# Kernel optimization log

Hardware: AMD Instinct MI355X
Metric: run time of the kernel (lower is better)

Reference implementation:

```python
import jax, jax.numpy as jnp
import numpy as np

N_NODES = 50000
N_EDGES = 800000
IN_CH = 64
HID = 128  # hidden_dim_conv == hidden_dim_readout


def setup_inputs() -> dict:
    key = jax.random.key(0)
    ks = jax.random.split(key, 16)
    x = jax.random.normal(ks[0], (N_NODES, 1, IN_CH), dtype=jnp.float32)
    edge_index = jax.random.randint(ks[1], (2, N_EDGES), 0, N_NODES, dtype=jnp.int64)
    edge_weight = jax.random.uniform(ks[2], (N_EDGES,), dtype=jnp.float32)

    def lin(k, out_d, in_d):
        s = 1.0 / np.sqrt(in_d)
        return jax.random.uniform(k, (out_d, in_d), minval=-s, maxval=s, dtype=jnp.float32)

    params = {
        "W_rel0": lin(ks[3], HID, IN_CH), "b_rel0": jnp.zeros((HID,), jnp.float32),
        "W_root0": lin(ks[4], HID, IN_CH),
        "W_ro0": lin(ks[5], HID, HID), "b_ro0": jnp.zeros((HID,), jnp.float32),
        "W_rel1": lin(ks[6], HID, HID), "b_rel1": jnp.zeros((HID,), jnp.float32),
        "W_root1": lin(ks[7], HID, HID),
        "W_ro1": lin(ks[8], HID, HID), "b_ro1": jnp.zeros((HID,), jnp.float32),
        "W_prd": lin(ks[9], 1, HID), "b_prd": jnp.zeros((1,), jnp.float32),
    }
    return {"dynamic_node_features": x, "edge_index": edge_index, "edge_weight": edge_weight, **params}


def reference(dynamic_node_features, edge_index, edge_weight,
              W_rel0, b_rel0, W_root0, W_ro0, b_ro0,
              W_rel1, b_rel1, W_root1, W_ro1, b_ro1,
              W_prd, b_prd):
    # Dropout layers are identity at inference.
    src, dst = edge_index[0], edge_index[1]
    n = dynamic_node_features.shape[0]
    # in-degree counts for 'mean' aggregation (nodes with no in-edges -> 0 output)
    counts = jax.ops.segment_sum(jnp.ones((edge_weight.shape[0],), edge_weight.dtype), dst, num_segments=n)
    denom = jnp.maximum(counts, 1.0)[:, None]  # [N,1]

    def graph_conv(h, W_rel, b_rel, W_root):
        # PyG GraphConv: lin_rel(mean_j edge_weight_ij * h_j) + lin_root(h_i)
        msg = edge_weight[:, None] * h[src]                       # [E,C]
        agg = jax.ops.segment_sum(msg, dst, num_segments=n) / denom  # [N,C]
        return agg @ W_rel.T + b_rel + h @ W_root.T

    h = dynamic_node_features[:, 0, :]                            # [N,IN_CH]
    h = jax.nn.relu(graph_conv(h, W_rel0, b_rel0, W_root0))
    h = jax.nn.relu(h @ W_ro0.T + b_ro0)                          # readout layer 0
    h = jax.nn.relu(graph_conv(h, W_rel1, b_rel1, W_root1))
    h = jax.nn.relu(h @ W_ro1.T + b_ro1)                          # readout layer 1
    out = h @ W_prd.T + b_prd                                     # [N,1]
    return out[:, None, :]                                        # [N,1,1]
```

## Files before the change

### kernel.cpp

```cpp
#include <hip/hip_runtime.h>
#include <hip/hip_fp16.h>

#define N_NODES 50000
#define N_EDGES 800000
#define IN_CH 64
#define HID 128
#define MAXDEG 64

typedef __attribute__((ext_vector_type(8))) short bf16x8;
typedef __attribute__((ext_vector_type(4))) float f32x4;

__device__ __forceinline__ unsigned pack_split(float v) {
    unsigned u = __float_as_uint(v);
    unsigned hi = (u + 0x7fffu + ((u >> 16) & 1u)) & 0xffff0000u;
    float r = v - __uint_as_float(hi);
    unsigned ur = __float_as_uint(r);
    unsigned lo = ((ur + 0x7fffu + ((ur >> 16) & 1u)) >> 16) & 0xffffu;
    return hi | lo;
}


__global__ __launch_bounds__(256) void count_fill_pack(
    const int* __restrict__ src, const int* __restrict__ dst,
    const float* __restrict__ w, int* __restrict__ cnt, int2* __restrict__ csr, int e,
    const float* __restrict__ x, unsigned* __restrict__ xp, __half* __restrict__ xh, int nx,
    const float* __restrict__ w_rel0, const float* __restrict__ w_root0,
    const float* __restrict__ w_ro0, const float* __restrict__ w_rel1,
    const float* __restrict__ w_root1, const float* __restrict__ w_ro1,
    unsigned short* __restrict__ hi, unsigned short* __restrict__ lo) {
    int tid = blockIdx.x * blockDim.x + threadIdx.x;
    int i8 = tid * 8;
    if (i8 + 7 < e) {
        int4 d0 = *(const int4*)&dst[i8];
        int4 d1 = *(const int4*)&dst[i8 + 4];
        int4 s0 = *(const int4*)&src[i8];
        int4 s1 = *(const int4*)&src[i8 + 4];
        float4 w0 = *(const float4*)&w[i8];
        float4 w1 = *(const float4*)&w[i8 + 4];
        int dd[8] = {d0.x, d0.y, d0.z, d0.w, d1.x, d1.y, d1.z, d1.w};
        int ss[8] = {s0.x, s0.y, s0.z, s0.w, s1.x, s1.y, s1.z, s1.w};
        float ww[8] = {w0.x, w0.y, w0.z, w0.w, w1.x, w1.y, w1.z, w1.w};
        int rr[8];
#pragma unroll
        for (int q = 0; q < 8; ++q) rr[q] = atomicAdd(&cnt[dd[q]], 1);
#pragma unroll
        for (int q = 0; q < 8; ++q) {
            if (rr[q] < MAXDEG) {
                unsigned long long v =
                    ((unsigned long long)(unsigned)__float_as_uint(ww[q]) << 32) | (unsigned)ss[q];
                __builtin_nontemporal_store(
                    v, (unsigned long long*)&csr[(size_t)dd[q] * MAXDEG + rr[q]]);
            }
        }
    } else if (i8 < e) {
        for (int i = i8; i < e; ++i) {
            int d = dst[i];
            int r = atomicAdd(&cnt[d], 1);
            if (r < MAXDEG) {
                unsigned long long v =
                    ((unsigned long long)(unsigned)__float_as_uint(w[i]) << 32) | (unsigned)src[i];
                __builtin_nontemporal_store(
                    v, (unsigned long long*)&csr[(size_t)d * MAXDEG + r]);
            }
        }
    }
    if (tid < nx) {
        float v = x[tid];
        xp[tid] = pack_split(v);
        xh[tid] = __float2half(v);
    }
    if (tid < 81920) {
        const float* srcw;
        int li;
        if (tid < 8192) { srcw = w_rel0; li = tid; }
        else if (tid < 16384) { srcw = w_root0; li = tid - 8192; }
        else if (tid < 32768) { srcw = w_ro0; li = tid - 16384; }
        else if (tid < 49152) { srcw = w_rel1; li = tid - 32768; }
        else if (tid < 65536) { srcw = w_root1; li = tid - 49152; }
        else { srcw = w_ro1; li = tid - 65536; }
        unsigned p = pack_split(srcw[li]);
        hi[tid] = (unsigned short)(p >> 16);
        lo[tid] = (unsigned short)(p & 0xffffu);
    }
}


template <int T, int ROW_STRIDE>
__device__ __forceinline__ void agg_tier_h2(const __half2* __restrict__ h2,
                                            const int2* __restrict__ cp,
                                            int& e, int end, int sl,
                                            float& ax, float& ay) {
    for (; e + T <= end; e += T) {
        int2 p[T];
        __half2 v[T];
#pragma unroll
        for (int q = 0; q < T; ++q) p[q] = cp[e + q];
#pragma unroll
        for (int q = 0; q < T; ++q) v[q] = h2[(size_t)p[q].x * ROW_STRIDE + sl];
#pragma unroll
        for (int q = 0; q < T; ++q) {
            float wv = __int_as_float(p[q].y);
            float2 f = __half22float2(v[q]);
            ax += wv * f.x;
            ay += wv * f.y;
        }
    }
}

__global__ void aggregate64(const __half2* __restrict__ xh2, const int* __restrict__ cnt,
                            const int2* __restrict__ csr,
                            unsigned* __restrict__ agg, int n) {
    int tid = blockIdx.x * blockDim.x + threadIdx.x;
    int lane = tid & 63;
    int half = lane >> 5;
    int sl = lane & 31;
    int node = ((tid >> 6) << 1) + half;
    if (node >= n) return;
    int deg = cnt[node];
    int end = deg < MAXDEG ? deg : MAXDEG;
    float inv = 1.0f / fmaxf((float)deg, 1.0f);
    const int2* cp = csr + (size_t)node * MAXDEG;
    float ax = 0.0f, ay = 0.0f;
    int e = 0;
    agg_tier_h2<16, 32>(xh2, cp, e, end, sl, ax, ay);
    agg_tier_h2<8, 32>(xh2, cp, e, end, sl, ax, ay);
    agg_tier_h2<4, 32>(xh2, cp, e, end, sl, ax, ay);
    agg_tier_h2<1, 32>(xh2, cp, e, end, sl, ax, ay);
    uint2 o;
    o.x = pack_split(ax * inv);
    o.y = pack_split(ay * inv);
    ((uint2*)agg)[(size_t)node * 32 + sl] = o;
}

__global__ void aggregate128(const __half2* __restrict__ h2h, const int* __restrict__ cnt,
                             const int2* __restrict__ csr,
                             unsigned* __restrict__ agg, int n) {
    int lane = threadIdx.x & 63;
    int node = (int)((blockIdx.x * blockDim.x + threadIdx.x) >> 6);
    if (node >= n) return;
    node = __builtin_amdgcn_readfirstlane(node);
    int deg = cnt[node];
    int end = deg < MAXDEG ? deg : MAXDEG;
    float inv = 1.0f / fmaxf((float)deg, 1.0f);
    const int2* cp = csr + (size_t)node * MAXDEG;
    float ax = 0.0f, ay = 0.0f;
    int e = 0;
    agg_tier_h2<16, 64>(h2h, cp, e, end, lane, ax, ay);
    agg_tier_h2<8, 64>(h2h, cp, e, end, lane, ax, ay);
    agg_tier_h2<4, 64>(h2h, cp, e, end, lane, ax, ay);
    agg_tier_h2<1, 64>(h2h, cp, e, end, lane, ax, ay);
    uint2 o;
    o.x = pack_split(ax * inv);
    o.y = pack_split(ay * inv);
    ((uint2*)agg)[(size_t)node * 64 + lane] = o;
}


template <int K, int NMAT, bool RELU, int EMIT>
__global__ __launch_bounds__(256, 2) void gemm_mfma(
    const unsigned* __restrict__ A0,
    const unsigned short* __restrict__ W0Hi, const unsigned short* __restrict__ W0Lo,
    const unsigned* __restrict__ A1,
    const unsigned short* __restrict__ W1Hi, const unsigned short* __restrict__ W1Lo,
    const float* __restrict__ bias, void* __restrict__ Yv, __half* __restrict__ Yh,
    const float* __restrict__ pred_w, const float* __restrict__ pred_b,
    float* __restrict__ pred_out, int n) {
    constexpr int KS = K / 32;
    const int lane = (int)threadIdx.x & 63;
    const int wv = (int)threadIdx.x >> 6;
    const int col = lane & 15;
    const int quad = lane >> 4;

    bf16x8 wh[NMAT][2][KS], wl[NMAT][2][KS];
#pragma unroll
    for (int m = 0; m < NMAT; ++m) {
        const unsigned short* Whi = m ? W1Hi : W0Hi;
        const unsigned short* Wlo = m ? W1Lo : W0Lo;
#pragma unroll
        for (int tt = 0; tt < 2; ++tt) {
            const int j = (2 * wv + tt) * 16 + col;
#pragma unroll
            for (int ks = 0; ks < KS; ++ks) {
                const size_t wo = (size_t)j * K + ks * 32 + quad * 8;
                wh[m][tt][ks] = *(const bf16x8*)&Whi[wo];
                wl[m][tt][ks] = *(const bf16x8*)&Wlo[wo];
            }
        }
    }

    float bb[2], wpv[2];
#pragma unroll
    for (int tt = 0; tt < 2; ++tt) {
        bb[tt] = bias[(2 * wv + tt) * 16 + col];
        if constexpr (EMIT == 2) wpv[tt] = pred_w[(2 * wv + tt) * 16 + col];
    }

    const int ngroups = (n + 15) >> 4;
    for (int g = (int)blockIdx.x; g < ngroups; g += (int)gridDim.x) {
        const int m0 = g * 16;
        int arow = m0 + col;
        if (arow >= n) arow = n - 1;

        f32x4 acc[2];
#pragma unroll
        for (int tt = 0; tt < 2; ++tt) acc[tt] = (f32x4){0.f, 0.f, 0.f, 0.f};

#pragma unroll
        for (int m = 0; m < NMAT; ++m) {
            const unsigned* Ap = m ? A1 : A0;
#pragma unroll
            for (int ks = 0; ks < KS; ++ks) {
                const unsigned* ap = &Ap[(size_t)arow * K + ks * 32 + quad * 8];
                uint4 q0 = *(const uint4*)ap;
                uint4 q1 = *(const uint4*)(ap + 4);
                bf16x8 ahi, alo;
                ahi[0] = (short)(q0.x >> 16); alo[0] = (short)(q0.x & 0xffffu);
                ahi[1] = (short)(q0.y >> 16); alo[1] = (short)(q0.y & 0xffffu);
                ahi[2] = (short)(q0.z >> 16); alo[2] = (short)(q0.z & 0xffffu);
                ahi[3] = (short)(q0.w >> 16); alo[3] = (short)(q0.w & 0xffffu);
                ahi[4] = (short)(q1.x >> 16); alo[4] = (short)(q1.x & 0xffffu);
                ahi[5] = (short)(q1.y >> 16); alo[5] = (short)(q1.y & 0xffffu);
                ahi[6] = (short)(q1.z >> 16); alo[6] = (short)(q1.z & 0xffffu);
                ahi[7] = (short)(q1.w >> 16); alo[7] = (short)(q1.w & 0xffffu);
#pragma unroll
                for (int tt = 0; tt < 2; ++tt) {
                    acc[tt] = __builtin_amdgcn_mfma_f32_16x16x32_bf16(ahi, wh[m][tt][ks], acc[tt], 0, 0, 0);
                    acc[tt] = __builtin_amdgcn_mfma_f32_16x16x32_bf16(ahi, wl[m][tt][ks], acc[tt], 0, 0, 0);
                    acc[tt] = __builtin_amdgcn_mfma_f32_16x16x32_bf16(alo, wh[m][tt][ks], acc[tt], 0, 0, 0);
                }
            }
        }

        float yv[2][4];
#pragma unroll
        for (int tt = 0; tt < 2; ++tt)
#pragma unroll
            for (int r = 0; r < 4; ++r) {
                float y = acc[tt][r] + bb[tt];
                if (RELU) y = fmaxf(y, 0.f);
                yv[tt][r] = y;
            }

        if constexpr (EMIT != 2) {
#pragma unroll
            for (int tt = 0; tt < 2; ++tt) {
                const int j = (2 * wv + tt) * 16 + col;
#pragma unroll
                for (int r = 0; r < 4; ++r) {
                    int node = m0 + quad * 4 + r;
                    if (node >= n) continue;
                    ((unsigned*)Yv)[(size_t)node * 128 + j] = pack_split(yv[tt][r]);
                    if constexpr (EMIT == 1)
                        Yh[(size_t)node * 128 + j] = __float2half(yv[tt][r]);
                }
            }
        } else {
            __shared__ float pp[4][16];
            float pr[4];
#pragma unroll
            for (int r = 0; r < 4; ++r) pr[r] = yv[0][r] * wpv[0] + yv[1][r] * wpv[1];
#pragma unroll
            for (int off = 8; off > 0; off >>= 1)
#pragma unroll
                for (int r = 0; r < 4; ++r) pr[r] += __shfl_down(pr[r], off);
            if (col == 0) {
#pragma unroll
                for (int r = 0; r < 4; ++r) pp[wv][quad * 4 + r] = pr[r];
            }
            __syncthreads();
            if (wv == 0 && lane < 16) {
                int node = m0 + lane;
                if (node < n)
                    pred_out[node] = pp[0][lane] + pp[1][lane] + pp[2][lane] + pp[3][lane] + pred_b[0];
            }
            __syncthreads();
        }
    }
}


extern "C" void kernel_launch(void* const* d_in, const int* in_sizes, int n_in,
                              void* d_out, int out_size, void* d_ws, size_t ws_size,
                              hipStream_t stream) {
    const float* x = (const float*)d_in[0];
    const int* edge_index = (const int*)d_in[1];
    const float* edge_w = (const float*)d_in[2];
    const float* W_rel0 = (const float*)d_in[3];
    const float* b_rel0 = (const float*)d_in[4];
    const float* W_root0 = (const float*)d_in[5];
    const float* W_ro0 = (const float*)d_in[6];
    const float* b_ro0 = (const float*)d_in[7];
    const float* W_rel1 = (const float*)d_in[8];
    const float* b_rel1 = (const float*)d_in[9];
    const float* W_root1 = (const float*)d_in[10];
    const float* W_ro1 = (const float*)d_in[11];
    const float* b_ro1 = (const float*)d_in[12];
    const float* W_prd = (const float*)d_in[13];
    const float* b_prd = (const float*)d_in[14];
    float* out = (float*)d_out;

    const int* e_src = edge_index;
    const int* e_dst = edge_index + N_EDGES;

    char* ws = (char*)d_ws;
    size_t off = 0;
    auto alloc = [&](size_t bytes) {
        char* p = ws + off;
        off += (bytes + 255) & ~(size_t)255;
        return p;
    };
    int* cnt = (int*)alloc(N_NODES * 4);
    int2* csr = (int2*)alloc((size_t)N_NODES * MAXDEG * 8);
    unsigned short* WHI = (unsigned short*)alloc(81920 * 2);
    unsigned short* WLO = (unsigned short*)alloc(81920 * 2);
    unsigned* xp = (unsigned*)alloc((size_t)N_NODES * 64 * 4);
    __half* xh = (__half*)alloc((size_t)N_NODES * 64 * 2);
    unsigned* AGGp = (unsigned*)alloc((size_t)N_NODES * 128 * 4);
    unsigned* B1p = (unsigned*)alloc((size_t)N_NODES * 128 * 4);
    unsigned* B2p = (unsigned*)alloc((size_t)N_NODES * 128 * 4);
    __half* H2h = (__half*)alloc((size_t)N_NODES * 128 * 2);

    hipMemsetAsync(cnt, 0, N_NODES * 4, stream);

    const int NX = N_NODES * 64;
    count_fill_pack<<<(NX + 255) / 256, 256, 0, stream>>>(
        e_src, e_dst, edge_w, cnt, csr, N_EDGES,
        x, xp, xh, NX, W_rel0, W_root0, W_ro0, W_rel1, W_root1, W_ro1, WHI, WLO);

    const int AGGB64 = (((N_NODES + 1) / 2) * 64 + 255) / 256;
    const int AGGB = (N_NODES * 64 + 255) / 256;
    const int GGRID = 512;

    aggregate64<<<AGGB64, 256, 0, stream>>>((const __half2*)xh, cnt, csr, AGGp, N_NODES);
    gemm_mfma<64, 2, true, 0><<<GGRID, 256, 0, stream>>>(
        AGGp, WHI + 0, WLO + 0, xp, WHI + 8192, WLO + 8192, b_rel0,
        B1p, nullptr, nullptr, nullptr, nullptr, N_NODES);
    gemm_mfma<128, 1, true, 1><<<GGRID, 256, 0, stream>>>(
        B1p, WHI + 16384, WLO + 16384, nullptr, nullptr, nullptr, b_ro0,
        B2p, H2h, nullptr, nullptr, nullptr, N_NODES);
    aggregate128<<<AGGB, 256, 0, stream>>>((const __half2*)H2h, cnt, csr, AGGp, N_NODES);
    gemm_mfma<128, 2, true, 0><<<GGRID, 256, 0, stream>>>(
        AGGp, WHI + 32768, WLO + 32768, B2p, WHI + 49152, WLO + 49152, b_rel1,
        B1p, nullptr, nullptr, nullptr, nullptr, N_NODES);
    gemm_mfma<128, 1, true, 2><<<GGRID, 256, 0, stream>>>(
        B1p, WHI + 65536, WLO + 65536, nullptr, nullptr, nullptr, b_ro1,
        nullptr, nullptr, W_prd, b_prd, out, N_NODES);
}
```

Before: 291.7 us.

## Fuse graph-conv GEMM with readout GEMM via LDS and halve aggregate128 lanes

Each graph-conv GEMM and the readout GEMM that follows it now run in one kernel. The ReLU'd intermediate for each 16-row tile is written to shared memory in hi/lo split form and fed straight into a second MFMA pass, which removes the B1 round trip to global memory and two launches. aggregate128 now uses 32 lanes per node with 8-byte half loads and four accumulators, and its tier unrolling is simplified. The trade-offs are higher register pressure, since the second weight set stays resident and the min-blocks launch bound is dropped, plus extra block barriers per tile.

```diff
diff --git a/kernel.cpp b/kernel.cpp
--- a/kernel.cpp
+++ b/kernel.cpp
@@ -85,36 +85,13 @@
 }
 
 
-template <int T, int ROW_STRIDE>
-__device__ __forceinline__ void agg_tier_h2(const __half2* __restrict__ h2,
-                                            const int2* __restrict__ cp,
-                                            int& e, int end, int sl,
-                                            float& ax, float& ay) {
-    for (; e + T <= end; e += T) {
-        int2 p[T];
-        __half2 v[T];
-#pragma unroll
-        for (int q = 0; q < T; ++q) p[q] = cp[e + q];
-#pragma unroll
-        for (int q = 0; q < T; ++q) v[q] = h2[(size_t)p[q].x * ROW_STRIDE + sl];
-#pragma unroll
-        for (int q = 0; q < T; ++q) {
-            float wv = __int_as_float(p[q].y);
-            float2 f = __half22float2(v[q]);
-            ax += wv * f.x;
-            ay += wv * f.y;
-        }
-    }
-}
-
 __global__ void aggregate64(const __half2* __restrict__ xh2, const int* __restrict__ cnt,
                             const int2* __restrict__ csr,
                             unsigned* __restrict__ agg, int n) {
     int tid = blockIdx.x * blockDim.x + threadIdx.x;
     int lane = tid & 63;
-    int half = lane >> 5;
     int sl = lane & 31;
-    int node = ((tid >> 6) << 1) + half;
+    int node = ((tid >> 6) << 1) + (lane >> 5);
     if (node >= n) return;
     int deg = cnt[node];
     int end = deg < MAXDEG ? deg : MAXDEG;
@@ -122,56 +99,124 @@
     const int2* cp = csr + (size_t)node * MAXDEG;
     float ax = 0.0f, ay = 0.0f;
     int e = 0;
-    agg_tier_h2<16, 32>(xh2, cp, e, end, sl, ax, ay);
-    agg_tier_h2<8, 32>(xh2, cp, e, end, sl, ax, ay);
-    agg_tier_h2<4, 32>(xh2, cp, e, end, sl, ax, ay);
-    agg_tier_h2<1, 32>(xh2, cp, e, end, sl, ax, ay);
+    for (; e + 16 <= end; e += 16) {
+        int2 p[16];
+        __half2 v[16];
+#pragma unroll
+        for (int q = 0; q < 16; ++q) p[q] = cp[e + q];
+#pragma unroll
+        for (int q = 0; q < 16; ++q) v[q] = xh2[(size_t)p[q].x * 32 + sl];
+#pragma unroll
+        for (int q = 0; q < 16; ++q) {
+            float wv = __int_as_float(p[q].y);
+            float2 f = __half22float2(v[q]);
+            ax += wv * f.x;
+            ay += wv * f.y;
+        }
+    }
+    for (; e + 4 <= end; e += 4) {
+        int2 p[4];
+        __half2 v[4];
+#pragma unroll
+        for (int q = 0; q < 4; ++q) p[q] = cp[e + q];
+#pragma unroll
+        for (int q = 0; q < 4; ++q) v[q] = xh2[(size_t)p[q].x * 32 + sl];
+#pragma unroll
+        for (int q = 0; q < 4; ++q) {
+            float wv = __int_as_float(p[q].y);
+            float2 f = __half22float2(v[q]);
+            ax += wv * f.x;
+            ay += wv * f.y;
+        }
+    }
+    for (; e < end; ++e) {
+        int2 p = cp[e];
+        float wv = __int_as_float(p.y);
+        float2 f = __half22float2(xh2[(size_t)p.x * 32 + sl]);
+        ax += wv * f.x;
+        ay += wv * f.y;
+    }
     uint2 o;
     o.x = pack_split(ax * inv);
     o.y = pack_split(ay * inv);
     ((uint2*)agg)[(size_t)node * 32 + sl] = o;
 }
 
-__global__ void aggregate128(const __half2* __restrict__ h2h, const int* __restrict__ cnt,
+__global__ void aggregate128(const uint2* __restrict__ h2h, const int* __restrict__ cnt,
                              const int2* __restrict__ csr,
                              unsigned* __restrict__ agg, int n) {
-    int lane = threadIdx.x & 63;
-    int node = (int)((blockIdx.x * blockDim.x + threadIdx.x) >> 6);
+    int tid = blockIdx.x * blockDim.x + threadIdx.x;
+    int lane = tid & 63;
+    int sl = lane & 31;
+    int node = ((tid >> 6) << 1) + (lane >> 5);
     if (node >= n) return;
-    node = __builtin_amdgcn_readfirstlane(node);
     int deg = cnt[node];
     int end = deg < MAXDEG ? deg : MAXDEG;
     float inv = 1.0f / fmaxf((float)deg, 1.0f);
     const int2* cp = csr + (size_t)node * MAXDEG;
-    float ax = 0.0f, ay = 0.0f;
+    float ax = 0.0f, ay = 0.0f, az = 0.0f, aw = 0.0f;
     int e = 0;
-    agg_tier_h2<16, 64>(h2h, cp, e, end, lane, ax, ay);
-    agg_tier_h2<8, 64>(h2h, cp, e, end, lane, ax, ay);
-    agg_tier_h2<4, 64>(h2h, cp, e, end, lane, ax, ay);
-    agg_tier_h2<1, 64>(h2h, cp, e, end, lane, ax, ay);
-    uint2 o;
+    for (; e + 8 <= end; e += 8) {
+        int2 p[8];
+        uint2 v[8];
+#pragma unroll
+        for (int q = 0; q < 8; ++q) p[q] = cp[e + q];
+#pragma unroll
+        for (int q = 0; q < 8; ++q) v[q] = h2h[(size_t)p[q].x * 32 + sl];
+#pragma unroll
+        for (int q = 0; q < 8; ++q) {
+            float wv = __int_as_float(p[q].y);
+            float2 f0 = __half22float2(*(const __half2*)&v[q].x);
+            float2 f1 = __half22float2(*(const __half2*)&v[q].y);
+            ax += wv * f0.x;
+            ay += wv * f0.y;
+            az += wv * f1.x;
+            aw += wv * f1.y;
+        }
+    }
+    for (; e < end; ++e) {
+        int2 p = cp[e];
+        float wv = __int_as_float(p.y);
+        uint2 v = h2h[(size_t)p.x * 32 + sl];
+        float2 f0 = __half22float2(*(const __half2*)&v.x);
+        float2 f1 = __half22float2(*(const __half2*)&v.y);
+        ax += wv * f0.x;
+        ay += wv * f0.y;
+        az += wv * f1.x;
+        aw += wv * f1.y;
+    }
+    uint4 o;
     o.x = pack_split(ax * inv);
     o.y = pack_split(ay * inv);
-    ((uint2*)agg)[(size_t)node * 64 + lane] = o;
-}
-
-
-template <int K, int NMAT, bool RELU, int EMIT>
-__global__ __launch_bounds__(256, 2) void gemm_mfma(
+    o.z = pack_split(az * inv);
+    o.w = pack_split(aw * inv);
+    *(uint4*)&agg[(size_t)node * 128 + sl * 4] = o;
+}
+
+
+template <int K1, int NMAT, int EMIT2>
+__global__ __launch_bounds__(256) void gemm_fused(
     const unsigned* __restrict__ A0,
     const unsigned short* __restrict__ W0Hi, const unsigned short* __restrict__ W0Lo,
     const unsigned* __restrict__ A1,
     const unsigned short* __restrict__ W1Hi, const unsigned short* __restrict__ W1Lo,
-    const float* __restrict__ bias, void* __restrict__ Yv, __half* __restrict__ Yh,
+    const float* __restrict__ bias1,
+    const unsigned short* __restrict__ W2Hi, const unsigned short* __restrict__ W2Lo,
+    const float* __restrict__ bias2,
+    void* __restrict__ Yv, __half* __restrict__ Yh,
     const float* __restrict__ pred_w, const float* __restrict__ pred_b,
     float* __restrict__ pred_out, int n) {
-    constexpr int KS = K / 32;
+    constexpr int KS1 = K1 / 32;
+    constexpr int KS2 = 128 / 32;
     const int lane = (int)threadIdx.x & 63;
     const int wv = (int)threadIdx.x >> 6;
     const int col = lane & 15;
     const int quad = lane >> 4;
 
-    bf16x8 wh[NMAT][2][KS], wl[NMAT][2][KS];
+    __shared__ unsigned h1s[16][132];
+    __shared__ float pp[4][16];
+
+    bf16x8 wh1[NMAT][2][KS1], wl1[NMAT][2][KS1];
 #pragma unroll
     for (int m = 0; m < NMAT; ++m) {
         const unsigned short* Whi = m ? W1Hi : W0Hi;
@@ -180,19 +225,31 @@
         for (int tt = 0; tt < 2; ++tt) {
             const int j = (2 * wv + tt) * 16 + col;
 #pragma unroll
-            for (int ks = 0; ks < KS; ++ks) {
-                const size_t wo = (size_t)j * K + ks * 32 + quad * 8;
-                wh[m][tt][ks] = *(const bf16x8*)&Whi[wo];
-                wl[m][tt][ks] = *(const bf16x8*)&Wlo[wo];
-            }
-        }
-    }
-
-    float bb[2], wpv[2];
+            for (int ks = 0; ks < KS1; ++ks) {
+                const size_t wo = (size_t)j * K1 + ks * 32 + quad * 8;
+                wh1[m][tt][ks] = *(const bf16x8*)&Whi[wo];
+                wl1[m][tt][ks] = *(const bf16x8*)&Wlo[wo];
+            }
+        }
+    }
+    bf16x8 wh2[2][KS2], wl2[2][KS2];
 #pragma unroll
     for (int tt = 0; tt < 2; ++tt) {
-        bb[tt] = bias[(2 * wv + tt) * 16 + col];
-        if constexpr (EMIT == 2) wpv[tt] = pred_w[(2 * wv + tt) * 16 + col];
+        const int j = (2 * wv + tt) * 16 + col;
+#pragma unroll
+        for (int ks = 0; ks < KS2; ++ks) {
+            const size_t wo = (size_t)j * 128 + ks * 32 + quad * 8;
+            wh2[tt][ks] = *(const bf16x8*)&W2Hi[wo];
+            wl2[tt][ks] = *(const bf16x8*)&W2Lo[wo];
+        }
+    }
+
+    float bb1[2], bb2[2], wpv[2];
+#pragma unroll
+    for (int tt = 0; tt < 2; ++tt) {
+        bb1[tt] = bias1[(2 * wv + tt) * 16 + col];
+        bb2[tt] = bias2[(2 * wv + tt) * 16 + col];
+        if constexpr (EMIT2 == 2) wpv[tt] = pred_w[(2 * wv + tt) * 16 + col];
     }
 
     const int ngroups = (n + 15) >> 4;
@@ -204,13 +261,12 @@
         f32x4 acc[2];
 #pragma unroll
         for (int tt = 0; tt < 2; ++tt) acc[tt] = (f32x4){0.f, 0.f, 0.f, 0.f};
-
 #pragma unroll
         for (int m = 0; m < NMAT; ++m) {
             const unsigned* Ap = m ? A1 : A0;
 #pragma unroll
-            for (int ks = 0; ks < KS; ++ks) {
-                const unsigned* ap = &Ap[(size_t)arow * K + ks * 32 + quad * 8];
+            for (int ks = 0; ks < KS1; ++ks) {
+                const unsigned* ap = &Ap[(size_t)arow * K1 + ks * 32 + quad * 8];
                 uint4 q0 = *(const uint4*)ap;
                 uint4 q1 = *(const uint4*)(ap + 4);
                 bf16x8 ahi, alo;
@@ -224,24 +280,54 @@
                 ahi[7] = (short)(q1.w >> 16); alo[7] = (short)(q1.w & 0xffffu);
 #pragma unroll
                 for (int tt = 0; tt < 2; ++tt) {
-                    acc[tt] = __builtin_amdgcn_mfma_f32_16x16x32_bf16(ahi, wh[m][tt][ks], acc[tt], 0, 0, 0);
-                    acc[tt] = __builtin_amdgcn_mfma_f32_16x16x32_bf16(ahi, wl[m][tt][ks], acc[tt], 0, 0, 0);
-                    acc[tt] = __builtin_amdgcn_mfma_f32_16x16x32_bf16(alo, wh[m][tt][ks], acc[tt], 0, 0, 0);
+                    acc[tt] = __builtin_amdgcn_mfma_f32_16x16x32_bf16(ahi, wh1[m][tt][ks], acc[tt], 0, 0, 0);
+                    acc[tt] = __builtin_amdgcn_mfma_f32_16x16x32_bf16(ahi, wl1[m][tt][ks], acc[tt], 0, 0, 0);
+                    acc[tt] = __builtin_amdgcn_mfma_f32_16x16x32_bf16(alo, wh1[m][tt][ks], acc[tt], 0, 0, 0);
                 }
             }
         }
+#pragma unroll
+        for (int tt = 0; tt < 2; ++tt)
+#pragma unroll
+            for (int r = 0; r < 4; ++r) {
+                float y = fmaxf(acc[tt][r] + bb1[tt], 0.f);
+                h1s[quad * 4 + r][(2 * wv + tt) * 16 + col] = pack_split(y);
+            }
+        __syncthreads();
+
+        f32x4 acc2[2];
+#pragma unroll
+        for (int tt = 0; tt < 2; ++tt) acc2[tt] = (f32x4){0.f, 0.f, 0.f, 0.f};
+#pragma unroll
+        for (int ks = 0; ks < KS2; ++ks) {
+            const uint4* lp = (const uint4*)&h1s[col][ks * 32 + quad * 8];
+            uint4 q0 = lp[0];
+            uint4 q1 = lp[1];
+            bf16x8 ahi, alo;
+            ahi[0] = (short)(q0.x >> 16); alo[0] = (short)(q0.x & 0xffffu);
+            ahi[1] = (short)(q0.y >> 16); alo[1] = (short)(q0.y & 0xffffu);
+            ahi[2] = (short)(q0.z >> 16); alo[2] = (short)(q0.z & 0xffffu);
+            ahi[3] = (short)(q0.w >> 16); alo[3] = (short)(q0.w & 0xffffu);
+            ahi[4] = (short)(q1.x >> 16); alo[4] = (short)(q1.x & 0xffffu);
+            ahi[5] = (short)(q1.y >> 16); alo[5] = (short)(q1.y & 0xffffu);
+            ahi[6] = (short)(q1.z >> 16); alo[6] = (short)(q1.z & 0xffffu);
+            ahi[7] = (short)(q1.w >> 16); alo[7] = (short)(q1.w & 0xffffu);
+#pragma unroll
+            for (int tt = 0; tt < 2; ++tt) {
+                acc2[tt] = __builtin_amdgcn_mfma_f32_16x16x32_bf16(ahi, wh2[tt][ks], acc2[tt], 0, 0, 0);
+                acc2[tt] = __builtin_amdgcn_mfma_f32_16x16x32_bf16(ahi, wl2[tt][ks], acc2[tt], 0, 0, 0);
+                acc2[tt] = __builtin_amdgcn_mfma_f32_16x16x32_bf16(alo, wh2[tt][ks], acc2[tt], 0, 0, 0);
+            }
+        }
 
         float yv[2][4];
 #pragma unroll
         for (int tt = 0; tt < 2; ++tt)
 #pragma unroll
-            for (int r = 0; r < 4; ++r) {
-                float y = acc[tt][r] + bb[tt];
-                if (RELU) y = fmaxf(y, 0.f);
-                yv[tt][r] = y;
-            }
-
-        if constexpr (EMIT != 2) {
+            for (int r = 0; r < 4; ++r)
+                yv[tt][r] = fmaxf(acc2[tt][r] + bb2[tt], 0.f);
+
+        if constexpr (EMIT2 == 1) {
 #pragma unroll
             for (int tt = 0; tt < 2; ++tt) {
                 const int j = (2 * wv + tt) * 16 + col;
@@ -250,12 +336,10 @@
                     int node = m0 + quad * 4 + r;
                     if (node >= n) continue;
                     ((unsigned*)Yv)[(size_t)node * 128 + j] = pack_split(yv[tt][r]);
-                    if constexpr (EMIT == 1)
-                        Yh[(size_t)node * 128 + j] = __float2half(yv[tt][r]);
+                    Yh[(size_t)node * 128 + j] = __float2half(yv[tt][r]);
                 }
             }
         } else {
-            __shared__ float pp[4][16];
             float pr[4];
 #pragma unroll
             for (int r = 0; r < 4; ++r) pr[r] = yv[0][r] * wpv[0] + yv[1][r] * wpv[1];
@@ -273,8 +357,8 @@
                 if (node < n)
                     pred_out[node] = pp[0][lane] + pp[1][lane] + pp[2][lane] + pp[3][lane] + pred_b[0];
             }
-            __syncthreads();
-        }
+        }
+        __syncthreads();
     }
 }
 
@@ -316,7 +400,6 @@
     unsigned* xp = (unsigned*)alloc((size_t)N_NODES * 64 * 4);
     __half* xh = (__half*)alloc((size_t)N_NODES * 64 * 2);
     unsigned* AGGp = (unsigned*)alloc((size_t)N_NODES * 128 * 4);
-    unsigned* B1p = (unsigned*)alloc((size_t)N_NODES * 128 * 4);
     unsigned* B2p = (unsigned*)alloc((size_t)N_NODES * 128 * 4);
     __half* H2h = (__half*)alloc((size_t)N_NODES * 128 * 2);
 
@@ -327,22 +410,17 @@
         e_src, e_dst, edge_w, cnt, csr, N_EDGES,
         x, xp, xh, NX, W_rel0, W_root0, W_ro0, W_rel1, W_root1, W_ro1, WHI, WLO);
 
-    const int AGGB64 = (((N_NODES + 1) / 2) * 64 + 255) / 256;
-    const int AGGB = (N_NODES * 64 + 255) / 256;
+    const int AGGB2 = (((N_NODES + 1) / 2) * 64 + 255) / 256;
     const int GGRID = 512;
 
-    aggregate64<<<AGGB64, 256, 0, stream>>>((const __half2*)xh, cnt, csr, AGGp, N_NODES);
-    gemm_mfma<64, 2, true, 0><<<GGRID, 256, 0, stream>>>(
+    aggregate64<<<AGGB2, 256, 0, stream>>>((const __half2*)xh, cnt, csr, AGGp, N_NODES);
+    gemm_fused<64, 2, 1><<<GGRID, 256, 0, stream>>>(
         AGGp, WHI + 0, WLO + 0, xp, WHI + 8192, WLO + 8192, b_rel0,
-        B1p, nullptr, nullptr, nullptr, nullptr, N_NODES);
-    gemm_mfma<128, 1, true, 1><<<GGRID, 256, 0, stream>>>(
-        B1p, WHI + 16384, WLO + 16384, nullptr, nullptr, nullptr, b_ro0,
+        WHI + 16384, WLO + 16384, b_ro0,
         B2p, H2h, nullptr, nullptr, nullptr, N_NODES);
-    aggregate128<<<AGGB, 256, 0, stream>>>((const __half2*)H2h, cnt, csr, AGGp, N_NODES);
-    gemm_mfma<128, 2, true, 0><<<GGRID, 256, 0, stream>>>(
+    aggregate128<<<AGGB2, 256, 0, stream>>>((const uint2*)H2h, cnt, csr, AGGp, N_NODES);
+    gemm_fused<128, 2, 2><<<GGRID, 256, 0, stream>>>(
         AGGp, WHI + 32768, WLO + 32768, B2p, WHI + 49152, WLO + 49152, b_rel1,
-        B1p, nullptr, nullptr, nullptr, nullptr, N_NODES);
-    gemm_mfma<128, 1, true, 2><<<GGRID, 256, 0, stream>>>(
-        B1p, WHI + 65536, WLO + 65536, nullptr, nullptr, nullptr, b_ro1,
+        WHI + 65536, WLO + 65536, b_ro1,
         nullptr, nullptr, W_prd, b_prd, out, N_NODES);
 }
```

After: 279.4 us. 1.04x faster.
